# Optimization experiments

Hardware: AMD Instinct MI355X
Metric: run time of the kernel (lower is better)

Reference implementation:

```python
import jax, jax.numpy as jnp
import numpy as np

N = 50000       # nodes
E = 800000      # edges (avg degree 16)
C_IN = 128
C_OUT = 64
C_HID = 2 * C_OUT  # 128, per Dir_Encoder_GCN


def gcn_conv(x, W, b, src, dst, ew, n):
    """PyG GCNConv: add self-loops (weight 1), symmetric normalization,
    aggregate transformed source features at destination, add bias."""
    loops = jnp.arange(n)
    s = jnp.concatenate([src, loops])                       # [E+N]
    d = jnp.concatenate([dst, loops])                       # [E+N]
    w = jnp.concatenate([ew, jnp.ones((n,), ew.dtype)])     # [E+N]
    deg = jax.ops.segment_sum(w, d, num_segments=n)         # weighted in-degree
    dinv = jnp.where(deg > 0, jax.lax.rsqrt(deg), 0.0)      # deg^{-1/2}
    norm = dinv[s] * w * dinv[d]                            # [E+N]
    xw = x @ W                                              # [n, out]
    out = jax.ops.segment_sum(xw[s] * norm[:, None], d, num_segments=n)
    return out + b


def setup_inputs() -> dict:
    key = jax.random.key(0)
    k1, k2, k3, k4, k5, k6, k7 = jax.random.split(key, 7)
    x = jax.random.normal(k1, (N, C_IN), dtype=jnp.float32)
    edge_index = jax.random.randint(k2, (2, E), 0, N, dtype=jnp.int64)
    edge_weight = jax.random.uniform(k3, (E,), dtype=jnp.float32)
    W1 = jax.random.normal(k4, (C_IN, C_HID), dtype=jnp.float32) * (1.0 / np.sqrt(C_IN))
    b1 = jnp.zeros((C_HID,), dtype=jnp.float32)
    W2 = jax.random.normal(k5, (C_HID, C_OUT), dtype=jnp.float32) * (1.0 / np.sqrt(C_HID))
    b2 = jnp.zeros((C_OUT,), dtype=jnp.float32)
    return {"x": x, "edge_index": edge_index, "edge_weight": edge_weight,
            "W1": W1, "b1": b1, "W2": W2, "b2": b2}


def reference(x, edge_index, edge_weight, W1, b1, W2, b2):
    src, dst = edge_index[0], edge_index[1]
    n = x.shape[0]
    h = jax.nn.elu(gcn_conv(x, W1, b1, src, dst, edge_weight, n))
    return jax.nn.softplus(gcn_conv(h, W2, b2, src, dst, edge_weight, n)) + 1e-4
```

## Files before the change

### kernel.cpp

```cpp
#include <hip/hip_runtime.h>
#include <math.h>

constexpr int CAP    = 48;
constexpr int CAPP   = 49;
constexpr int SEGCAP = 4608;
constexpr int CE     = 3136;


__device__ __forceinline__ uint f2bf(float f) {
    union { float f; uint i; } v; v.f = f;
    uint r = v.i + 0x7FFFu + ((v.i >> 16) & 1u);
    return r >> 16;
}
__device__ __forceinline__ void bf8_expand(uint4 q, float* o) {
    uint u[4] = {q.x, q.y, q.z, q.w};
#pragma unroll
    for (int j = 0; j < 4; ++j) {
        union { uint i; float f; } lo, hi;
        lo.i = u[j] << 16;
        hi.i = u[j] & 0xFFFF0000u;
        o[2 * j] = lo.f;
        o[2 * j + 1] = hi.f;
    }
}


__global__ __launch_bounds__(256) void k_p1(const int* __restrict__ src,
                                            const int* __restrict__ dst,
                                            const float* __restrict__ ew,
                                            int* __restrict__ g_bin_cnt,
                                            int2* __restrict__ seg, int E) {
    __shared__ int hist[256];
    __shared__ int base[256];
    const int tid = threadIdx.x;
    const int e0 = blockIdx.x * CE;
    const int e1 = min(e0 + CE, E);

    hist[tid] = 0;
    __syncthreads();
    for (int e = e0 + tid; e < e1; e += 256) atomicAdd(&hist[dst[e] >> 8], 1);
    __syncthreads();
    base[tid] = (hist[tid] > 0) ? atomicAdd(&g_bin_cnt[tid], hist[tid]) : 0;
    __syncthreads();
    hist[tid] = 0;
    __syncthreads();
    for (int e = e0 + tid; e < e1; e += 256) {
        int d = dst[e];
        int b = d >> 8;
        int r = atomicAdd(&hist[b], 1);
        int slot = base[b] + r;
        if (slot < SEGCAP)
            seg[(size_t)b * SEGCAP + slot] =
                make_int2(((d & 255) << 16) | src[e], __float_as_int(ew[e]));
    }
}


__global__ __launch_bounds__(256) void k_p2(const int* __restrict__ g_bin_cnt,
                                            const int2* __restrict__ seg,
                                            int* __restrict__ cnt, float* __restrict__ dinv,
                                            int2* __restrict__ bucket, int N) {
    __shared__ int2 lb[256 * CAPP];
    __shared__ int lcnt[256];
    __shared__ float ldeg[256];
    const int b = blockIdx.x;
    const int tid = threadIdx.x;
    lcnt[tid] = 0;
    ldeg[tid] = 0.f;
    __syncthreads();

    const int m = min(g_bin_cnt[b], SEGCAP);
    const int2* s = seg + (size_t)b * SEGCAP;
    for (int i = tid; i < m; i += 256) {
        int2 p = s[i];
        int dl = (p.x >> 16) & 255;
        int sv = p.x & 0xFFFF;
        int slot = atomicAdd(&lcnt[dl], 1);
        if (slot < CAP) lb[dl * CAPP + slot] = make_int2(sv, p.y);
        atomicAdd(&ldeg[dl], __int_as_float(p.y));
    }
    __syncthreads();

    const int node0 = b * 256;
    int node = node0 + tid;
    if (node < N) {
        cnt[node] = min(lcnt[tid], CAP);
        dinv[node] = rsqrtf(1.0f + ldeg[tid]);
    }
    const int nn = min(256, N - node0);
    for (int i = tid; i < nn * CAP; i += 256) {
        int nl = i / CAP;
        int j = i - nl * CAP;
        bucket[((size_t)node0 + nl) * CAP + j] = lb[nl * CAPP + j];
    }
}


template <int COLS, typename TIN>
__global__ __launch_bounds__(256) void k_gemm(const TIN* __restrict__ X,
                                              const float* __restrict__ W,
                                              ushort* __restrict__ Y, int n) {
    constexpr int K = 128;
    constexpr int KC = 32;
    constexpr int XS = 132;
    constexpr int TGX = COLS / 4;
    constexpr int TM = (64 * TGX) / 256;
    __shared__ float xs[64 * XS];
    __shared__ float ws[KC * COLS];

    const int tid = threadIdx.x;
    const int r0 = blockIdx.x * 64;

    if constexpr (sizeof(TIN) == 4) {
        for (int i = tid * 4; i < 64 * K; i += 1024) {
            int row = i >> 7;
            int col = i & 127;
            int g = r0 + row;
            float4 v = make_float4(0.f, 0.f, 0.f, 0.f);
            if (g < n) v = *(const float4*)((const float*)X + (size_t)g * K + col);
            *(float4*)(xs + row * XS + col) = v;
        }
    } else {
        for (int i = tid; i < 64 * 16; i += 256) {
            int row = i >> 4;
            int ko = (i & 15) * 8;
            int g = r0 + row;
            float f[8] = {0.f, 0.f, 0.f, 0.f, 0.f, 0.f, 0.f, 0.f};
            if (g < n) {
                uint4 q = *(const uint4*)((const ushort*)X + (size_t)g * K + ko);
                bf8_expand(q, f);
            }
            *(float4*)(xs + row * XS + ko) = make_float4(f[0], f[1], f[2], f[3]);
            *(float4*)(xs + row * XS + ko + 4) = make_float4(f[4], f[5], f[6], f[7]);
        }
    }

    const int tx = tid % TGX;
    const int ty = tid / TGX;

    float acc[TM][4];
#pragma unroll
    for (int r = 0; r < TM; r++) acc[r][0] = acc[r][1] = acc[r][2] = acc[r][3] = 0.f;

    const float* xrow = xs + (ty * TM) * XS;
    for (int kc = 0; kc < K; kc += KC) {
        __syncthreads();
        for (int i = tid; i < (KC * COLS) / 4; i += 256)
            *(float4*)(ws + i * 4) = *(const float4*)(W + kc * COLS + i * 4);
        __syncthreads();
#pragma unroll 4
        for (int kk = 0; kk < KC; ++kk) {
            float4 w4 = *(const float4*)(ws + kk * COLS + tx * 4);
            const float* xr = xrow + kc + kk;
#pragma unroll
            for (int r = 0; r < TM; ++r) {
                float xv = xr[r * XS];
                acc[r][0] += xv * w4.x;
                acc[r][1] += xv * w4.y;
                acc[r][2] += xv * w4.z;
                acc[r][3] += xv * w4.w;
            }
        }
    }

#pragma unroll
    for (int r = 0; r < TM; ++r) {
        int g = r0 + ty * TM + r;
        if (g < n) {
            ushort4 o;
            o.x = (ushort)f2bf(acc[r][0]);
            o.y = (ushort)f2bf(acc[r][1]);
            o.z = (ushort)f2bf(acc[r][2]);
            o.w = (ushort)f2bf(acc[r][3]);
            *(ushort4*)(Y + (size_t)g * COLS + tx * 4) = o;
        }
    }
}


template <int C, int ACT>
__global__ __launch_bounds__(256) void k_gather(const ushort* __restrict__ xw,
                                                const float* __restrict__ dinv,
                                                const float* __restrict__ b,
                                                const int* __restrict__ cnt,
                                                const int2* __restrict__ bucket,
                                                void* __restrict__ outv, int n) {
    constexpr int L = C / 8;
    constexpr int GPB = 256 / L;
    int node = blockIdx.x * GPB + threadIdx.x / L;
    int lane = threadIdx.x % L;
    if (node >= n) return;

    float dd = dinv[node];
    float acc[8];
    {
        float4 b0 = *(const float4*)(b + lane * 8);
        float4 b1 = *(const float4*)(b + lane * 8 + 4);
        float sf[8];
        uint4 q = *(const uint4*)(xw + (size_t)node * C + lane * 8);
        bf8_expand(q, sf);
        float s2 = dd * dd;
        acc[0] = b0.x + sf[0] * s2;
        acc[1] = b0.y + sf[1] * s2;
        acc[2] = b0.z + sf[2] * s2;
        acc[3] = b0.w + sf[3] * s2;
        acc[4] = b1.x + sf[4] * s2;
        acc[5] = b1.y + sf[5] * s2;
        acc[6] = b1.z + sf[6] * s2;
        acc[7] = b1.w + sf[7] * s2;
    }

    int c = min(cnt[node], CAP);
    const int2* bk = bucket + (size_t)node * CAP;

    int i = 0;
    for (; i + 4 <= c; i += 4) {
        int4 p0 = *(const int4*)(bk + i);
        int4 p1 = *(const int4*)(bk + i + 2);
        float w0 = dinv[p0.x] * __int_as_float(p0.y) * dd;
        float w1 = dinv[p0.z] * __int_as_float(p0.w) * dd;
        float w2 = dinv[p1.x] * __int_as_float(p1.y) * dd;
        float w3 = dinv[p1.z] * __int_as_float(p1.w) * dd;
        uint4 q0 = *(const uint4*)(xw + (size_t)p0.x * C + lane * 8);
        uint4 q1 = *(const uint4*)(xw + (size_t)p0.z * C + lane * 8);
        uint4 q2 = *(const uint4*)(xw + (size_t)p1.x * C + lane * 8);
        uint4 q3 = *(const uint4*)(xw + (size_t)p1.z * C + lane * 8);
        float f[8];
        bf8_expand(q0, f);
#pragma unroll
        for (int j = 0; j < 8; ++j) acc[j] += f[j] * w0;
        bf8_expand(q1, f);
#pragma unroll
        for (int j = 0; j < 8; ++j) acc[j] += f[j] * w1;
        bf8_expand(q2, f);
#pragma unroll
        for (int j = 0; j < 8; ++j) acc[j] += f[j] * w2;
        bf8_expand(q3, f);
#pragma unroll
        for (int j = 0; j < 8; ++j) acc[j] += f[j] * w3;
    }
    for (; i < c; ++i) {
        int2 sw = bk[i];
        float w = dinv[sw.x] * __int_as_float(sw.y) * dd;
        uint4 q = *(const uint4*)(xw + (size_t)sw.x * C + lane * 8);
        float f[8];
        bf8_expand(q, f);
#pragma unroll
        for (int j = 0; j < 8; ++j) acc[j] += f[j] * w;
    }

    if (ACT == 0) {
#pragma unroll
        for (int j = 0; j < 8; ++j) acc[j] = acc[j] > 0.f ? acc[j] : expm1f(acc[j]);
        uint4 o;
        o.x = f2bf(acc[0]) | (f2bf(acc[1]) << 16);
        o.y = f2bf(acc[2]) | (f2bf(acc[3]) << 16);
        o.z = f2bf(acc[4]) | (f2bf(acc[5]) << 16);
        o.w = f2bf(acc[6]) | (f2bf(acc[7]) << 16);
        *(uint4*)((ushort*)outv + (size_t)node * C + lane * 8) = o;
    } else {
#pragma unroll
        for (int j = 0; j < 8; ++j)
            acc[j] = ((acc[j] > 20.f) ? acc[j] : log1pf(expf(acc[j]))) + 1e-4f;
        float* out = (float*)outv;
        *(float4*)(out + (size_t)node * C + lane * 8) =
            make_float4(acc[0], acc[1], acc[2], acc[3]);
        *(float4*)(out + (size_t)node * C + lane * 8 + 4) =
            make_float4(acc[4], acc[5], acc[6], acc[7]);
    }
}


extern "C" void kernel_launch(void* const* d_in, const int* in_sizes, int n_in,
                              void* d_out, int out_size, void* d_ws, size_t ws_size,
                              hipStream_t stream) {
    const float* x  = (const float*)d_in[0];
    const int*   ei = (const int*)d_in[1];
    const float* ew = (const float*)d_in[2];
    const float* W1 = (const float*)d_in[3];
    const float* b1 = (const float*)d_in[4];
    const float* W2 = (const float*)d_in[5];
    const float* b2 = (const float*)d_in[6];

    const int N = in_sizes[0] / 128;
    const int E = in_sizes[1] / 2;
    const int* src = ei;
    const int* dst = ei + E;
    float* y = (float*)d_out;

    const int nbins = (N + 255) >> 8;

    char* p = (char*)d_ws;
    auto take = [&](size_t bytes) {
        char* q = p;
        p += (bytes + 255) & ~(size_t)255;
        return q;
    };

    int*    g_bin_cnt = (int*)take(256 * 4);
    int2*   seg       = (int2*)take((size_t)nbins * SEGCAP * 8);
    int*    cnt       = (int*)take((size_t)N * 4);
    float*  dinv      = (float*)take((size_t)N * 4);
    int2*   bucket    = (int2*)take((size_t)N * CAP * 8);
    ushort* xw        = (ushort*)take((size_t)N * 128 * 2);
    ushort* h         = (ushort*)take((size_t)N * 128 * 2);
    ushort* hw        = (ushort*)take((size_t)N * 64 * 2);

    auto cdiv = [](int a, int b) { return (a + b - 1) / b; };

    hipMemsetAsync(g_bin_cnt, 0, 256 * 4, stream);
    k_p1<<<cdiv(E, CE), 256, 0, stream>>>(src, dst, ew, g_bin_cnt, seg, E);
    k_p2<<<nbins, 256, 0, stream>>>(g_bin_cnt, seg, cnt, dinv, bucket, N);

    k_gemm<128, float><<<cdiv(N, 64), 256, 0, stream>>>(x, W1, xw, N);
    k_gather<128, 0><<<cdiv(N, 16), 256, 0, stream>>>(xw, dinv, b1, cnt, bucket, h, N);
    k_gemm<64, ushort><<<cdiv(N, 64), 256, 0, stream>>>(h, W2, hw, N);
    k_gather<64, 1><<<cdiv(N, 32), 256, 0, stream>>>(hw, dinv, b2, cnt, bucket, y, N);
}
```

Baseline: 225.1 us.

## Replace scalar FP32 GEMMs with bf16 MFMA using hi/lo split precision

Both dense feature transforms now run on MFMA 16x16x32 bf16 instructions instead of shared-memory FP32 FMA loops. The weights are first packed into the MFMA operand layout by a small kernel, which also splits each value into bf16 hi and lo parts. FP32 inputs are split the same way, so three MFMA products roughly recover FP32 accuracy. This targets compute-bound GEMM time, at the cost of extra MFMA work, two extra tiny launches, and uncoalesced scalar ushort output stores.

```diff
diff --git a/kernel.cpp b/kernel.cpp
--- a/kernel.cpp
+++ b/kernel.cpp
@@ -6,11 +6,18 @@
 constexpr int SEGCAP = 4608;
 constexpr int CE     = 3136;
 
+typedef short v8s __attribute__((ext_vector_type(8)));
+typedef float v4f __attribute__((ext_vector_type(4)));
+
 
 __device__ __forceinline__ uint f2bf(float f) {
     union { float f; uint i; } v; v.f = f;
     uint r = v.i + 0x7FFFu + ((v.i >> 16) & 1u);
     return r >> 16;
+}
+__device__ __forceinline__ float bf2f(uint h) {
+    union { uint i; float f; } v; v.i = h << 16;
+    return v.f;
 }
 __device__ __forceinline__ void bf8_expand(uint4 q, float* o) {
     uint u[4] = {q.x, q.y, q.z, q.w};
@@ -96,83 +103,87 @@
 }
 
 
-template <int COLS, typename TIN>
-__global__ __launch_bounds__(256) void k_gemm(const TIN* __restrict__ X,
-                                              const float* __restrict__ W,
-                                              ushort* __restrict__ Y, int n) {
-    constexpr int K = 128;
-    constexpr int KC = 32;
-    constexpr int XS = 132;
-    constexpr int TGX = COLS / 4;
-    constexpr int TM = (64 * TGX) / 256;
-    __shared__ float xs[64 * XS];
-    __shared__ float ws[KC * COLS];
-
-    const int tid = threadIdx.x;
-    const int r0 = blockIdx.x * 64;
-
-    if constexpr (sizeof(TIN) == 4) {
-        for (int i = tid * 4; i < 64 * K; i += 1024) {
-            int row = i >> 7;
-            int col = i & 127;
-            int g = r0 + row;
-            float4 v = make_float4(0.f, 0.f, 0.f, 0.f);
-            if (g < n) v = *(const float4*)((const float*)X + (size_t)g * K + col);
-            *(float4*)(xs + row * XS + col) = v;
+template <int COLS>
+__global__ __launch_bounds__(256) void k_pack(const float* __restrict__ W,
+                                              ushort* __restrict__ wpk) {
+    constexpr int NT = COLS / 16;
+    int id = blockIdx.x * 256 + threadIdx.x;
+    if (id >= 4 * NT * 64) return;
+    int lane = id & 63;
+    int t = (id >> 6) % NT;
+    int c = (id >> 6) / NT;
+    int ncol = t * 16 + (lane & 15);
+    int k0 = c * 32 + (lane >> 4) * 8;
+    ushort hi[8], lo[8];
+#pragma unroll
+    for (int j = 0; j < 8; ++j) {
+        float v = W[(size_t)(k0 + j) * COLS + ncol];
+        ushort h = (ushort)f2bf(v);
+        hi[j] = h;
+        lo[j] = (ushort)f2bf(v - bf2f(h));
+    }
+    size_t bh = ((size_t)(c * NT + t) * 64 + lane) * 8;
+    size_t bl = ((size_t)((4 + c) * NT + t) * 64 + lane) * 8;
+    *(uint4*)(wpk + bh) = *(uint4*)hi;
+    *(uint4*)(wpk + bl) = *(uint4*)lo;
+}
+
+
+template <int COLS, bool FP32IN>
+__global__ __launch_bounds__(256) void k_gemm_mfma(const void* __restrict__ Xv,
+                                                   const ushort* __restrict__ wpk,
+                                                   ushort* __restrict__ Y, int n) {
+    constexpr int NT = COLS / 16;
+    const int wave = threadIdx.x >> 6;
+    const int lane = threadIdx.x & 63;
+    const int m = lane & 15;
+    const int q = lane >> 4;
+    const int r0 = blockIdx.x * 64 + wave * 16;
+
+    v4f acc[NT];
+#pragma unroll
+    for (int t = 0; t < NT; ++t) acc[t] = (v4f){0.f, 0.f, 0.f, 0.f};
+
+    const int arow = min(r0 + m, n - 1);
+
+    for (int c = 0; c < 4; ++c) {
+        v8s a_hi, a_lo;
+        if (FP32IN) {
+            const float* xp = (const float*)Xv + (size_t)arow * 128 + c * 32 + q * 8;
+            float4 v0 = *(const float4*)xp;
+            float4 v1 = *(const float4*)(xp + 4);
+            float f[8] = {v0.x, v0.y, v0.z, v0.w, v1.x, v1.y, v1.z, v1.w};
+            union { ushort u[8]; v8s v; } H, L;
+#pragma unroll
+            for (int j = 0; j < 8; ++j) {
+                ushort h = (ushort)f2bf(f[j]);
+                H.u[j] = h;
+                L.u[j] = (ushort)f2bf(f[j] - bf2f(h));
+            }
+            a_hi = H.v;
+            a_lo = L.v;
+        } else {
+            const ushort* xp = (const ushort*)Xv + (size_t)arow * 128 + c * 32 + q * 8;
+            a_hi = *(const v8s*)xp;
         }
-    } else {
-        for (int i = tid; i < 64 * 16; i += 256) {
-            int row = i >> 4;
-            int ko = (i & 15) * 8;
-            int g = r0 + row;
-            float f[8] = {0.f, 0.f, 0.f, 0.f, 0.f, 0.f, 0.f, 0.f};
-            if (g < n) {
-                uint4 q = *(const uint4*)((const ushort*)X + (size_t)g * K + ko);
-                bf8_expand(q, f);
-            }
-            *(float4*)(xs + row * XS + ko) = make_float4(f[0], f[1], f[2], f[3]);
-            *(float4*)(xs + row * XS + ko + 4) = make_float4(f[4], f[5], f[6], f[7]);
+#pragma unroll
+        for (int t = 0; t < NT; ++t) {
+            v8s b_hi = *(const v8s*)(wpk + ((size_t)(c * NT + t) * 64 + lane) * 8);
+            v8s b_lo = *(const v8s*)(wpk + ((size_t)((4 + c) * NT + t) * 64 + lane) * 8);
+            acc[t] = __builtin_amdgcn_mfma_f32_16x16x32_bf16(a_hi, b_hi, acc[t], 0, 0, 0);
+            acc[t] = __builtin_amdgcn_mfma_f32_16x16x32_bf16(a_hi, b_lo, acc[t], 0, 0, 0);
+            if (FP32IN)
+                acc[t] = __builtin_amdgcn_mfma_f32_16x16x32_bf16(a_lo, b_hi, acc[t], 0, 0, 0);
         }
     }
 
-    const int tx = tid % TGX;
-    const int ty = tid / TGX;
-
-    float acc[TM][4];
-#pragma unroll
-    for (int r = 0; r < TM; r++) acc[r][0] = acc[r][1] = acc[r][2] = acc[r][3] = 0.f;
-
-    const float* xrow = xs + (ty * TM) * XS;
-    for (int kc = 0; kc < K; kc += KC) {
-        __syncthreads();
-        for (int i = tid; i < (KC * COLS) / 4; i += 256)
-            *(float4*)(ws + i * 4) = *(const float4*)(W + kc * COLS + i * 4);
-        __syncthreads();
-#pragma unroll 4
-        for (int kk = 0; kk < KC; ++kk) {
-            float4 w4 = *(const float4*)(ws + kk * COLS + tx * 4);
-            const float* xr = xrow + kc + kk;
-#pragma unroll
-            for (int r = 0; r < TM; ++r) {
-                float xv = xr[r * XS];
-                acc[r][0] += xv * w4.x;
-                acc[r][1] += xv * w4.y;
-                acc[r][2] += xv * w4.z;
-                acc[r][3] += xv * w4.w;
-            }
-        }
-    }
-
-#pragma unroll
-    for (int r = 0; r < TM; ++r) {
-        int g = r0 + ty * TM + r;
-        if (g < n) {
-            ushort4 o;
-            o.x = (ushort)f2bf(acc[r][0]);
-            o.y = (ushort)f2bf(acc[r][1]);
-            o.z = (ushort)f2bf(acc[r][2]);
-            o.w = (ushort)f2bf(acc[r][3]);
-            *(ushort4*)(Y + (size_t)g * COLS + tx * 4) = o;
+#pragma unroll
+    for (int r = 0; r < 4; ++r) {
+        int row = r0 + q * 4 + r;
+        if (row < n) {
+#pragma unroll
+            for (int t = 0; t < NT; ++t)
+                Y[(size_t)row * COLS + t * 16 + m] = (ushort)f2bf(acc[t][r]);
         }
     }
 }
@@ -305,15 +316,19 @@
     ushort* xw        = (ushort*)take((size_t)N * 128 * 2);
     ushort* h         = (ushort*)take((size_t)N * 128 * 2);
     ushort* hw        = (ushort*)take((size_t)N * 64 * 2);
+    ushort* wpk1      = (ushort*)take(2 * 4 * 8 * 64 * 8 * 2);
+    ushort* wpk2      = (ushort*)take(2 * 4 * 4 * 64 * 8 * 2);
 
     auto cdiv = [](int a, int b) { return (a + b - 1) / b; };
 
     hipMemsetAsync(g_bin_cnt, 0, 256 * 4, stream);
     k_p1<<<cdiv(E, CE), 256, 0, stream>>>(src, dst, ew, g_bin_cnt, seg, E);
+    k_pack<128><<<8, 256, 0, stream>>>(W1, wpk1);
+    k_pack<64><<<4, 256, 0, stream>>>(W2, wpk2);
     k_p2<<<nbins, 256, 0, stream>>>(g_bin_cnt, seg, cnt, dinv, bucket, N);
 
-    k_gemm<128, float><<<cdiv(N, 64), 256, 0, stream>>>(x, W1, xw, N);
+    k_gemm_mfma<128, true><<<cdiv(N, 64), 256, 0, stream>>>(x, wpk1, xw, N);
     k_gather<128, 0><<<cdiv(N, 16), 256, 0, stream>>>(xw, dinv, b1, cnt, bucket, h, N);
-    k_gemm<64, ushort><<<cdiv(N, 64), 256, 0, stream>>>(h, W2, hw, N);
+    k_gemm_mfma<64, false><<<cdiv(N, 64), 256, 0, stream>>>(h, wpk2, hw, N);
     k_gather<64, 1><<<cdiv(N, 32), 256, 0, stream>>>(hw, dinv, b2, cnt, bucket, y, N);
 }
```

New measurement: 199.3 us. 11.4% less time.
